# Kernel optimization log

Measured on AMD Instinct MI355X. Metric: run time of the kernel, lower is better.

## Reference

```python
import jax, jax.numpy as jnp
import numpy as np

D = 256; HEADS = 8; DH = D // HEADS; LEVELS = 4; POINTS = 4; NLAYERS = 6; DFF = 1024
SHAPES = ((92, 160), (46, 80), (23, 40), (12, 20))  # (H, W) per level
LEN = sum(h * w for h, w in SHAPES)  # 19560
BS = 4; NQ = 900; EPS = 1e-5
SCALE = 1.0 / float(np.sqrt(DH))


def setup_inputs() -> dict:
    ks = iter(jax.random.split(jax.random.key(0), 64))
    def rn(shape, s=0.02):
        return jax.random.normal(next(ks), shape, jnp.float32) * s
    inp = {}
    inp['tgt'] = jax.random.normal(next(ks), (BS, NQ, D), jnp.float32)
    inp['reference_points'] = jax.random.uniform(next(ks), (BS, NQ, 3), jnp.float32)
    inp['src'] = jax.random.normal(next(ks), (BS, LEN, D), jnp.float32)
    inp['valid_ratios'] = jnp.ones((BS, LEVELS, 2), jnp.float32)
    inp['query_pos'] = jax.random.normal(next(ks), (BS, NQ, D), jnp.float32)
    # per-layer stacked parameters [NLAYERS, ...]
    inp['sa_in_w'] = rn((NLAYERS, 3 * D, D)); inp['sa_in_b'] = jnp.zeros((NLAYERS, 3 * D))
    inp['sa_out_w'] = rn((NLAYERS, D, D)); inp['sa_out_b'] = jnp.zeros((NLAYERS, D))
    inp['samp_w'] = rn((NLAYERS, HEADS * LEVELS * POINTS * 2, D), 0.01)
    inp['samp_b'] = jax.random.uniform(next(ks), (NLAYERS, HEADS * LEVELS * POINTS * 2), jnp.float32, -2.0, 2.0)
    inp['attn_w'] = rn((NLAYERS, HEADS * LEVELS * POINTS, D)); inp['attn_b'] = jnp.zeros((NLAYERS, HEADS * LEVELS * POINTS))
    inp['val_w'] = rn((NLAYERS, D, D)); inp['val_b'] = jnp.zeros((NLAYERS, D))
    inp['ca_out_w'] = rn((NLAYERS, D, D)); inp['ca_out_b'] = jnp.zeros((NLAYERS, D))
    inp['ffn1_w'] = rn((NLAYERS, DFF, D)); inp['ffn1_b'] = jnp.zeros((NLAYERS, DFF))
    inp['ffn2_w'] = rn((NLAYERS, D, DFF)); inp['ffn2_b'] = jnp.zeros((NLAYERS, D))
    for i in (1, 2, 3):
        inp['ln%d_w' % i] = jnp.ones((NLAYERS, D)); inp['ln%d_b' % i] = jnp.zeros((NLAYERS, D))
    return inp


def _ln(x, w, b):
    mu = x.mean(-1, keepdims=True)
    var = ((x - mu) ** 2).mean(-1, keepdims=True)
    return (x - mu) / jnp.sqrt(var + EPS) * w + b


def _self_attn(q, k, v, in_w, in_b, out_w, out_b):
    wq, wk, wv = jnp.split(in_w, 3, 0)
    bq, bk, bv = jnp.split(in_b, 3, 0)
    def proj(x, w, b):
        return (x @ w.T + b).reshape(BS, -1, HEADS, DH).transpose(0, 2, 1, 3)
    qh, kh, vh = proj(q, wq, bq), proj(k, wk, bk), proj(v, wv, bv)
    att = jax.nn.softmax(jnp.einsum('bhqd,bhkd->bhqk', qh * SCALE, kh), axis=-1)
    o = jnp.einsum('bhqk,bhkd->bhqd', att, vh).transpose(0, 2, 1, 3).reshape(BS, -1, D)
    return o @ out_w.T + out_b


def _msda(query, ref, src, sw, sb, aw, ab, vw, vb, ow, ob):
    # query [bs,NQ,D]; ref [bs,NQ,LEVELS,2] normalized xz coords
    value = (src @ vw.T + vb).reshape(BS, LEN, HEADS, DH)
    off = (query @ sw.T + sb).reshape(BS, NQ, HEADS, LEVELS, POINTS, 2)
    attn = jax.nn.softmax((query @ aw.T + ab).reshape(BS, NQ, HEADS, LEVELS * POINTS), -1)
    attn = attn.reshape(BS, NQ, HEADS, LEVELS, POINTS)
    norm = jnp.asarray([[w, h] for h, w in SHAPES], jnp.float32)  # (W,H) per level
    loc = ref[:, :, None, :, None, :] + off / norm[None, None, None, :, None, :]
    out = jnp.zeros((BS, HEADS, NQ, DH), jnp.float32)
    start = 0
    for l, (H, W) in enumerate(SHAPES):
        v_l = value[:, start:start + H * W].transpose(0, 2, 1, 3)  # [bs,heads,HW,dh]
        start += H * W
        ll = loc[:, :, :, l]  # [bs,NQ,heads,P,2]
        x = ll[..., 0] * W - 0.5
        y = ll[..., 1] * H - 0.5
        x0 = jnp.floor(x); y0 = jnp.floor(y)
        fx = x - x0; fy = y - y0
        x0i = x0.astype(jnp.int32); y0i = y0.astype(jnp.int32)
        def gather(xi, yi):
            inb = ((xi >= 0) & (xi < W) & (yi >= 0) & (yi < H)).astype(jnp.float32)
            idx = jnp.clip(yi, 0, H - 1) * W + jnp.clip(xi, 0, W - 1)
            idxt = idx.transpose(0, 2, 1, 3).reshape(BS, HEADS, NQ * POINTS, 1)
            g = jnp.take_along_axis(v_l, idxt, axis=2).reshape(BS, HEADS, NQ, POINTS, DH)
            return g * inb.transpose(0, 2, 1, 3)[..., None]
        def wt(w4):
            return w4.transpose(0, 2, 1, 3)[..., None]
        samp = (gather(x0i, y0i) * wt((1 - fx) * (1 - fy))
                + gather(x0i + 1, y0i) * wt(fx * (1 - fy))
                + gather(x0i, y0i + 1) * wt((1 - fx) * fy)
                + gather(x0i + 1, y0i + 1) * wt(fx * fy))
        out = out + (samp * attn[:, :, :, l].transpose(0, 2, 1, 3)[..., None]).sum(3)
    out = out.transpose(0, 2, 1, 3).reshape(BS, NQ, D)
    return out @ ow.T + ob


def _forward(tgt, reference_points, src, valid_ratios, query_pos,
             sa_in_w, sa_in_b, sa_out_w, sa_out_b,
             samp_w, samp_b, attn_w, attn_b, val_w, val_b, ca_out_w, ca_out_b,
             ffn1_w, ffn1_b, ffn2_w, ffn2_b,
             ln1_w, ln1_b, ln2_w, ln2_b, ln3_w, ln3_b):
    # reference_points last dim == 3 (x,y,z); deformable attn uses (x,z)
    ref_xz = jnp.concatenate([reference_points[..., :1], reference_points[..., 2:]], -1)
    ref_in = ref_xz[:, :, None] * valid_ratios[:, None]  # [bs,NQ,LEVELS,2]
    out = tgt
    for l in range(NLAYERS):
        q = out + query_pos
        sa = _self_attn(q, q, out, sa_in_w[l], sa_in_b[l], sa_out_w[l], sa_out_b[l])
        out = _ln(out + sa, ln1_w[l], ln1_b[l])
        ca = _msda(out + query_pos, ref_in, src, samp_w[l], samp_b[l], attn_w[l], attn_b[l],
                   val_w[l], val_b[l], ca_out_w[l], ca_out_b[l])
        out = _ln(out + ca, ln2_w[l], ln2_b[l])
        h = jax.nn.relu(out @ ffn1_w[l].T + ffn1_b[l]) @ ffn2_w[l].T + ffn2_b[l]
        out = _ln(out + h, ln3_w[l], ln3_b[l])
    return out


def reference(tgt, reference_points, src, valid_ratios, query_pos,
              sa_in_w, sa_in_b, sa_out_w, sa_out_b,
              samp_w, samp_b, attn_w, attn_b, val_w, val_b, ca_out_w, ca_out_b,
              ffn1_w, ffn1_b, ffn2_w, ffn2_b,
              ln1_w, ln1_b, ln2_w, ln2_b, ln3_w, ln3_b):
    return _forward(tgt, reference_points, src, valid_ratios, query_pos,
                    sa_in_w, sa_in_b, sa_out_w, sa_out_b,
                    samp_w, samp_b, attn_w, attn_b, val_w, val_b, ca_out_w, ca_out_b,
                    ffn1_w, ffn1_b, ffn2_w, ffn2_b,
                    ln1_w, ln1_b, ln2_w, ln2_b, ln3_w, ln3_b)
```

## Files before the change

kernel.cpp:

```cpp
#include <hip/hip_runtime.h>
#include <math.h>

#define DMODEL 256
#define HEADS 8
#define DHEAD 32
#define LEVELS 4
#define POINTS 4
#define NLAYERS 6
#define DFF 1024
#define BS 4
#define NQ 900
#define SLEN 19560
#define EPS_LN 1e-5f
#define ATT_SCALE 0.17677669529663689f

typedef __attribute__((ext_vector_type(8))) short bf16x8;
typedef __attribute__((ext_vector_type(4))) float f32x4;
typedef __attribute__((ext_vector_type(4))) unsigned short u16x4;
typedef __attribute__((ext_vector_type(8))) unsigned short u16x8;

__device__ __forceinline__ unsigned short f2b(float x) {
  unsigned u = __float_as_uint(x);
  u += 0x7FFF + ((u >> 16) & 1);
  return (unsigned short)(u >> 16);
}
__device__ __forceinline__ float b2f(unsigned short v) {
  return __uint_as_float(((unsigned)v) << 16);
}

__global__ __launch_bounds__(256) void copycvt_k(const float* __restrict__ a,
                                                 const float* __restrict__ qp,
                                                 float* __restrict__ cf,
                                                 unsigned short* __restrict__ cb,
                                                 unsigned short* __restrict__ qb, int n4) {
  int i = blockIdx.x * 256 + threadIdx.x;
  if (i < n4) {
    float4 v = reinterpret_cast<const float4*>(a)[i];
    float4 q = reinterpret_cast<const float4*>(qp)[i];
    reinterpret_cast<float4*>(cf)[i] = v;
    u16x4 o4 = {f2b(v.x), f2b(v.y), f2b(v.z), f2b(v.w)};
    reinterpret_cast<u16x4*>(cb)[i] = o4;
    u16x4 p4 = {f2b(q.x), f2b(q.y), f2b(q.z), f2b(q.w)};
    reinterpret_cast<u16x4*>(qb)[i] = p4;
  }
}

#define N4_SRC (SLEN * BS * DMODEL / 4)
#define N4_SAIN (NLAYERS * 768 * 256 / 4)
#define N4_SQ (NLAYERS * 256 * 256 / 4)
#define N4_FFN (NLAYERS * DFF * 256 / 4)
__global__ __launch_bounds__(256) void f2ball_k(
    const float* __restrict__ s0, const float* __restrict__ s1,
    const float* __restrict__ s2, const float* __restrict__ s3,
    const float* __restrict__ s4, const float* __restrict__ s5,
    const float* __restrict__ s6,
    unsigned short* __restrict__ d0, unsigned short* __restrict__ d1,
    unsigned short* __restrict__ d2, unsigned short* __restrict__ d3,
    unsigned short* __restrict__ d4, unsigned short* __restrict__ d5,
    unsigned short* __restrict__ d6) {
  const int total = N4_SRC + N4_SAIN + 3 * N4_SQ + 2 * N4_FFN;
  for (int i = blockIdx.x * 256 + threadIdx.x; i < total; i += gridDim.x * 256) {
    const float* s;
    unsigned short* d;
    int j = i;
    if (j < N4_SRC) { s = s0; d = d0; }
    else { j -= N4_SRC;
      if (j < N4_SAIN) { s = s1; d = d1; }
      else { j -= N4_SAIN;
        if (j < N4_SQ) { s = s2; d = d2; }
        else { j -= N4_SQ;
          if (j < N4_SQ) { s = s3; d = d3; }
          else { j -= N4_SQ;
            if (j < N4_SQ) { s = s4; d = d4; }
            else { j -= N4_SQ;
              if (j < N4_FFN) { s = s5; d = d5; }
              else { j -= N4_FFN; s = s6; d = d6; } } } } } }
    float4 v = reinterpret_cast<const float4*>(s)[j];
    u16x4 o4 = {f2b(v.x), f2b(v.y), f2b(v.z), f2b(v.w)};
    reinterpret_cast<u16x4*>(d)[j] = o4;
  }
}

__global__ __launch_bounds__(256) void catw_k(const float* __restrict__ sw,
                                              const float* __restrict__ aw,
                                              const float* __restrict__ sb,
                                              const float* __restrict__ ab,
                                              unsigned short* __restrict__ wout,
                                              float* __restrict__ bout) {
  int i = blockIdx.x * 256 + threadIdx.x;
  const int total4 = NLAYERS * 384 * 256 / 4;
  if (i < total4) {
    int l = i / (384 * 64);
    int r = i % (384 * 64);
    int row = r / 64;
    int c4 = r % 64;
    const float* srcp = row < 256
        ? sw + ((size_t)l * 256 * 256 + (size_t)row * 256 + c4 * 4)
        : aw + ((size_t)l * 128 * 256 + (size_t)(row - 256) * 256 + c4 * 4);
    float4 v = *(const float4*)srcp;
    u16x4 o4 = {f2b(v.x), f2b(v.y), f2b(v.z), f2b(v.w)};
    *(u16x4*)(wout + (size_t)i * 4) = o4;
  }
  if (i < NLAYERS * 384) {
    int l = i / 384, r = i % 384;
    bout[i] = r < 256 ? sb[l * 256 + r] : ab[l * 128 + (r - 256)];
  }
}

__global__ __launch_bounds__(256) void stackqk_k(const float* __restrict__ w_in,
                                                 const float* __restrict__ b_in,
                                                 unsigned short* __restrict__ qkW,
                                                 float* __restrict__ bqk) {
  int i = blockIdx.x * 256 + threadIdx.x;
  const int total4 = NLAYERS * 512 * 256 / 4;
  if (i < total4) {
    int l = i / (512 * 64);
    int r = i % (512 * 64);
    int row = r / 64, c4 = r % 64;
    float4 v = *(const float4*)(w_in + (size_t)l * 768 * 256 + (size_t)row * 256 + c4 * 4);
    u16x4 o4 = {f2b(v.x), f2b(v.y), f2b(v.z), f2b(v.w)};
    *(u16x4*)(qkW + ((size_t)(l * 512 + row) * 256 + c4 * 4)) = o4;
  }
  if (i < NLAYERS * 512) {
    int l = i / 512, r = i % 512;
    bqk[i] = b_in[l * 768 + r];
  }
}

__global__ __launch_bounds__(256) void gemm_bf_k(const unsigned short* __restrict__ A,
                                                 const unsigned short* __restrict__ W,
                                                 const float* __restrict__ bias,
                                                 const float* __restrict__ res,
                                                 int res_n, int ldr,
                                                 float* __restrict__ outf,
                                                 unsigned short* __restrict__ outb,
                                                 int ldo, int M, int N, int K, int relu) {
  __shared__ unsigned short As[64][72];
  __shared__ unsigned short Ws[64][72];
  const int tid = threadIdx.x;
  const int lane = tid & 63, wv = tid >> 6;
  const int wm = wv >> 1, wn = wv & 1;
  const int m0 = blockIdx.x * 64, n0 = blockIdx.y * 64;
  const int l15 = lane & 15, l4 = lane >> 4;

  f32x4 acc[2][2] = {};
  for (int k0 = 0; k0 < K; k0 += 64) {
#pragma unroll
    for (int t = 0; t < 2; ++t) {
      int u = t * 256 + tid;
      int r = u >> 3, c8 = u & 7;
      int ra = m0 + r; if (ra >= M) ra = M - 1;
      *(u16x8*)&As[r][c8 * 8] = *(const u16x8*)(A + (size_t)ra * K + k0 + c8 * 8);
      *(u16x8*)&Ws[r][c8 * 8] = *(const u16x8*)(W + (size_t)(n0 + r) * K + k0 + c8 * 8);
    }
    __syncthreads();
#pragma unroll
    for (int ks = 0; ks < 64; ks += 32) {
      bf16x8 af[2], wf[2];
#pragma unroll
      for (int fr = 0; fr < 2; ++fr)
        af[fr] = *(const bf16x8*)&As[wm * 32 + fr * 16 + l15][ks + l4 * 8];
#pragma unroll
      for (int fn = 0; fn < 2; ++fn)
        wf[fn] = *(const bf16x8*)&Ws[wn * 32 + fn * 16 + l15][ks + l4 * 8];
#pragma unroll
      for (int fr = 0; fr < 2; ++fr)
#pragma unroll
        for (int fn = 0; fn < 2; ++fn)
          acc[fr][fn] = __builtin_amdgcn_mfma_f32_16x16x32_bf16(
              af[fr], wf[fn], acc[fr][fn], 0, 0, 0);
    }
    __syncthreads();
  }
#pragma unroll
  for (int fr = 0; fr < 2; ++fr)
#pragma unroll
    for (int fn = 0; fn < 2; ++fn) {
      int col = n0 + wn * 32 + fn * 16 + l15;
      float bs = bias[col];
#pragma unroll
      for (int j = 0; j < 4; ++j) {
        int row = m0 + wm * 32 + fr * 16 + l4 * 4 + j;
        if (row >= M) continue;
        float v = acc[fr][fn][j];
        if (res && col < res_n) v += res[(size_t)row * ldr + col];
        else v += bs;
        if (relu) v = fmaxf(v, 0.f);
        if (outf) outf[(size_t)row * ldo + col] = v;
        if (outb) outb[(size_t)row * ldo + col] = f2b(v);
      }
    }
}

__global__ __launch_bounds__(256) void gemm_lnres_k(const unsigned short* __restrict__ A,
                                                    const unsigned short* __restrict__ W,
                                                    const float* __restrict__ bias,
                                                    const float* __restrict__ res,
                                                    const float* __restrict__ lnw,
                                                    const float* __restrict__ lnb,
                                                    float* __restrict__ outf,
                                                    unsigned short* __restrict__ outb,
                                                    int M, int K) {
  __shared__ unsigned short As[32][72];
  __shared__ unsigned short Ws[256][72];
  __shared__ float Os[32][264];
  const int tid = threadIdx.x;
  const int lane = tid & 63, wv = tid >> 6;
  const int l15 = lane & 15, l4 = lane >> 4;
  const int m0 = blockIdx.x * 32;

  f32x4 acc[2][4] = {};
  for (int k0 = 0; k0 < K; k0 += 64) {
    {
      int r = tid >> 3, c8 = tid & 7;
      int ra = m0 + r; if (ra >= M) ra = M - 1;
      *(u16x8*)&As[r][c8 * 8] = *(const u16x8*)(A + (size_t)ra * K + k0 + c8 * 8);
#pragma unroll
      for (int t = 0; t < 8; ++t) {
        int u = t * 256 + tid;
        int wr = u >> 3, wc = u & 7;
        *(u16x8*)&Ws[wr][wc * 8] = *(const u16x8*)(W + (size_t)wr * K + k0 + wc * 8);
      }
    }
    __syncthreads();
#pragma unroll
    for (int ks = 0; ks < 64; ks += 32) {
      bf16x8 af[2], wf[4];
#pragma unroll
      for (int fr = 0; fr < 2; ++fr)
        af[fr] = *(const bf16x8*)&As[fr * 16 + l15][ks + l4 * 8];
#pragma unroll
      for (int fc = 0; fc < 4; ++fc)
        wf[fc] = *(const bf16x8*)&Ws[wv * 64 + fc * 16 + l15][ks + l4 * 8];
#pragma unroll
      for (int fr = 0; fr < 2; ++fr)
#pragma unroll
        for (int fc = 0; fc < 4; ++fc)
          acc[fr][fc] = __builtin_amdgcn_mfma_f32_16x16x32_bf16(
              af[fr], wf[fc], acc[fr][fc], 0, 0, 0);
    }
    __syncthreads();
  }
#pragma unroll
  for (int fr = 0; fr < 2; ++fr)
#pragma unroll
    for (int fc = 0; fc < 4; ++fc) {
      int col = wv * 64 + fc * 16 + l15;
      float bs = bias[col];
#pragma unroll
      for (int j = 0; j < 4; ++j) {
        int row = fr * 16 + l4 * 4 + j;
        int grow = m0 + row;
        float v = acc[fr][fc][j] + bs + (grow < M ? res[(size_t)grow * 256 + col] : 0.f);
        Os[row][col] = v;
      }
    }
  __syncthreads();
  float4 wv4 = *(const float4*)(lnw + lane * 4);
  float4 bv4 = *(const float4*)(lnb + lane * 4);
#pragma unroll
  for (int i = 0; i < 8; ++i) {
    int row = wv * 8 + i;
    int grow = m0 + row;
    float4 x = *(float4*)&Os[row][lane * 4];
    float s = x.x + x.y + x.z + x.w;
#pragma unroll
    for (int m = 1; m < 64; m <<= 1) s += __shfl_xor(s, m);
    const float mu = s * (1.f / DMODEL);
    float4 v = {x.x - mu, x.y - mu, x.z - mu, x.w - mu};
    float q = v.x * v.x + v.y * v.y + v.z * v.z + v.w * v.w;
#pragma unroll
    for (int m = 1; m < 64; m <<= 1) q += __shfl_xor(q, m);
    const float rstd = rsqrtf(q * (1.f / DMODEL) + EPS_LN);
    float4 y = {v.x * rstd * wv4.x + bv4.x, v.y * rstd * wv4.y + bv4.y,
                v.z * rstd * wv4.z + bv4.z, v.w * rstd * wv4.w + bv4.w};
    if (grow < M) {
      *(float4*)(outf + (size_t)grow * 256 + lane * 4) = y;
      if (outb) {
        u16x4 ob = {f2b(y.x), f2b(y.y), f2b(y.z), f2b(y.w)};
        *(u16x4*)(outb + (size_t)grow * 256 + lane * 4) = ob;
      }
    }
  }
}

__global__ __launch_bounds__(256) void gemm_vmfma_k(const unsigned short* __restrict__ A,
                                                    const unsigned short* __restrict__ W,
                                                    const float* __restrict__ bias,
                                                    unsigned short* __restrict__ C,
                                                    int M) {
  __shared__ unsigned short As[128][72];
  __shared__ unsigned short Ws[128][72];
  const int tid = threadIdx.x;
  const int lane = tid & 63, wv = tid >> 6;
  const int wm = wv >> 1, wn = wv & 1;
  const int m0 = blockIdx.x * 128, n0 = blockIdx.y * 128;
  const int l15 = lane & 15, l4 = lane >> 4;

  f32x4 acc[4][4] = {};

  for (int k0 = 0; k0 < 256; k0 += 64) {
#pragma unroll
    for (int t = 0; t < 4; ++t) {
      int u = t * 256 + tid;
      int r = u >> 3, c8 = u & 7;
      int ra = m0 + r; if (ra >= M) ra = M - 1;
      *(u16x8*)&As[r][c8 * 8] = *(const u16x8*)(A + (size_t)ra * 256 + k0 + c8 * 8);
      *(u16x8*)&Ws[r][c8 * 8] = *(const u16x8*)(W + (size_t)(n0 + r) * 256 + k0 + c8 * 8);
    }
    __syncthreads();
#pragma unroll
    for (int ks = 0; ks < 64; ks += 32) {
      bf16x8 af[4], bf[4];
#pragma unroll
      for (int fr = 0; fr < 4; ++fr)
        af[fr] = *(const bf16x8*)&As[wm * 64 + fr * 16 + l15][ks + l4 * 8];
#pragma unroll
      for (int fn = 0; fn < 4; ++fn)
        bf[fn] = *(const bf16x8*)&Ws[wn * 64 + fn * 16 + l15][ks + l4 * 8];
#pragma unroll
      for (int fr = 0; fr < 4; ++fr)
#pragma unroll
        for (int fn = 0; fn < 4; ++fn)
          acc[fr][fn] = __builtin_amdgcn_mfma_f32_16x16x32_bf16(
              af[fr], bf[fn], acc[fr][fn], 0, 0, 0);
    }
    __syncthreads();
  }
#pragma unroll
  for (int fr = 0; fr < 4; ++fr)
#pragma unroll
    for (int fn = 0; fn < 4; ++fn) {
      int col = n0 + wn * 64 + fn * 16 + l15;
      float bs = bias[col];
#pragma unroll
      for (int j = 0; j < 4; ++j) {
        int row = m0 + wm * 64 + fr * 16 + l4 * 4 + j;
        if (row < M) C[(size_t)row * 256 + col] = f2b(acc[fr][fn][j] + bs);
      }
    }
}

__global__ __launch_bounds__(256) void fattn_mfma_k(const unsigned short* __restrict__ qkv,
                                                    unsigned short* __restrict__ o) {
  __shared__ unsigned short Qlds[64][40];
  __shared__ unsigned short Klds[64][40];
  __shared__ unsigned short Vt[32][72];
  __shared__ unsigned short Plds[64][72];
  const int tid = threadIdx.x;
  const int lane = tid & 63;
  const int wq = tid >> 6;
  const int l15 = lane & 15, l4 = lane >> 4;
  const int q0 = blockIdx.x * 64;
  const int h = blockIdx.y, b = blockIdx.z;
  const int hq = h * 32;
  const size_t rowb = (size_t)b * NQ;

  {
    int q = q0 + (tid >> 2);
    int qc = q < NQ ? q : NQ - 1;
    *(u16x8*)&Qlds[tid >> 2][(tid & 3) * 8] =
        *(const u16x8*)(qkv + (rowb + qc) * 768 + hq + (tid & 3) * 8);
  }
  __syncthreads();
  const bf16x8 qf = *(const bf16x8*)&Qlds[wq * 16 + l15][l4 * 8];

  float m_r[4] = {-1e30f, -1e30f, -1e30f, -1e30f};
  float l_r[4] = {0.f, 0.f, 0.f, 0.f};
  f32x4 oacc[2] = {};

  for (int k0 = 0; k0 < NQ; k0 += 64) {
    __syncthreads();
    {
      int kk = k0 + (tid >> 2);
      int kc = kk < NQ ? kk : NQ - 1;
      const unsigned short* kbase = qkv + (rowb + kc) * 768 + hq + (tid & 3) * 8;
      u16x8 kv = *(const u16x8*)(kbase + 256);
      u16x8 vv = *(const u16x8*)(kbase + 512);
      *(u16x8*)&Klds[tid >> 2][(tid & 3) * 8] = kv;
#pragma unroll
      for (int i = 0; i < 8; ++i) Vt[(tid & 3) * 8 + i][tid >> 2] = vv[i];
    }
    __syncthreads();

    f32x4 s[4];
#pragma unroll
    for (int fc = 0; fc < 4; ++fc) {
      bf16x8 kf = *(const bf16x8*)&Klds[fc * 16 + l15][l4 * 8];
      s[fc] = __builtin_amdgcn_mfma_f32_16x16x32_bf16(qf, kf, (f32x4){0.f, 0.f, 0.f, 0.f}, 0, 0, 0);
    }
#pragma unroll
    for (int fc = 0; fc < 4; ++fc) {
      bool oob = (k0 + fc * 16 + l15) >= NQ;
#pragma unroll
      for (int j = 0; j < 4; ++j)
        s[fc][j] = oob ? -1e30f : s[fc][j] * ATT_SCALE;
    }
#pragma unroll
    for (int j = 0; j < 4; ++j) {
      float tm = fmaxf(fmaxf(s[0][j], s[1][j]), fmaxf(s[2][j], s[3][j]));
      tm = fmaxf(tm, __shfl_xor(tm, 1, 16));
      tm = fmaxf(tm, __shfl_xor(tm, 2, 16));
      tm = fmaxf(tm, __shfl_xor(tm, 4, 16));
      tm = fmaxf(tm, __shfl_xor(tm, 8, 16));
      float mn = fmaxf(m_r[j], tm);
      float sf = __expf(m_r[j] - mn);
      m_r[j] = mn;
      oacc[0][j] *= sf;
      oacc[1][j] *= sf;
      float rs = 0.f;
#pragma unroll
      for (int fc = 0; fc < 4; ++fc) {
        float pv = __expf(s[fc][j] - mn);
        s[fc][j] = pv;
        rs += pv;
      }
      rs += __shfl_xor(rs, 1, 16);
      rs += __shfl_xor(rs, 2, 16);
      rs += __shfl_xor(rs, 4, 16);
      rs += __shfl_xor(rs, 8, 16);
      l_r[j] = l_r[j] * sf + rs;
    }
#pragma unroll
    for (int fc = 0; fc < 4; ++fc)
#pragma unroll
      for (int j = 0; j < 4; ++j)
        Plds[wq * 16 + l4 * 4 + j][fc * 16 + l15] = f2b(s[fc][j]);
    __syncthreads();
#pragma unroll
    for (int ks = 0; ks < 2; ++ks) {
      bf16x8 pf = *(const bf16x8*)&Plds[wq * 16 + l15][ks * 32 + l4 * 8];
#pragma unroll
      for (int oc = 0; oc < 2; ++oc) {
        bf16x8 vf = *(const bf16x8*)&Vt[oc * 16 + l15][ks * 32 + l4 * 8];
        oacc[oc] = __builtin_amdgcn_mfma_f32_16x16x32_bf16(pf, vf, oacc[oc], 0, 0, 0);
      }
    }
  }
#pragma unroll
  for (int j = 0; j < 4; ++j) {
    int q = q0 + wq * 16 + l4 * 4 + j;
    if (q < NQ) {
      float inv = 1.f / l_r[j];
      o[(rowb + q) * 256 + hq + l15] = f2b(oacc[0][j] * inv);
      o[(rowb + q) * 256 + hq + 16 + l15] = f2b(oacc[1][j] * inv);
    }
  }
}

__global__ __launch_bounds__(256) void msda_k(const float* __restrict__ refp,
                                              const float* __restrict__ vr,
                                              const unsigned short* __restrict__ value,
                                              const float* __restrict__ cat,
                                              unsigned short* __restrict__ outp) {
  const int HW[4][2] = {{92, 160}, {46, 80}, {23, 40}, {12, 20}};
  const int START[4] = {0, 14720, 18400, 19320};
  const int qi = blockIdx.x, b = blockIdx.y;
  const int tid = threadIdx.x;
  const int h = tid >> 5;
  const int r = tid & 31;
  const int lvl = r >> 3;
  const int li = r & 7;
  const size_t base = (size_t)(b * NQ + qi);
  const float rx = refp[base * 3 + 0];
  const float rz = refp[base * 3 + 2];

  const float* lg = cat + base * 384 + 256 + h * 16;
  float4 L0 = *(const float4*)(lg + 0);
  float4 L1 = *(const float4*)(lg + 4);
  float4 L2 = *(const float4*)(lg + 8);
  float4 L3 = *(const float4*)(lg + 12);
  float mx = fmaxf(fmaxf(fmaxf(L0.x, L0.y), fmaxf(L0.z, L0.w)),
                   fmaxf(fmaxf(fmaxf(L1.x, L1.y), fmaxf(L1.z, L1.w)),
                         fmaxf(fmaxf(fmaxf(L2.x, L2.y), fmaxf(L2.z, L2.w)),
                               fmaxf(fmaxf(L3.x, L3.y), fmaxf(L3.z, L3.w)))));
  float4 E0 = {__expf(L0.x - mx), __expf(L0.y - mx), __expf(L0.z - mx), __expf(L0.w - mx)};
  float4 E1 = {__expf(L1.x - mx), __expf(L1.y - mx), __expf(L1.z - mx), __expf(L1.w - mx)};
  float4 E2 = {__expf(L2.x - mx), __expf(L2.y - mx), __expf(L2.z - mx), __expf(L2.w - mx)};
  float4 E3 = {__expf(L3.x - mx), __expf(L3.y - mx), __expf(L3.z - mx), __expf(L3.w - mx)};
  float sum = E0.x + E0.y + E0.z + E0.w + E1.x + E1.y + E1.z + E1.w +
              E2.x + E2.y + E2.z + E2.w + E3.x + E3.y + E3.z + E3.w;
  const float inv = 1.f / sum;
  float4 Emy = lvl == 0 ? E0 : lvl == 1 ? E1 : lvl == 2 ? E2 : E3;
  float wl[4] = {Emy.x * inv, Emy.y * inv, Emy.z * inv, Emy.w * inv};

  const int H = HW[lvl][0], W = HW[lvl][1];
  const float refx = rx * vr[(b * LEVELS + lvl) * 2 + 0] * (float)W;
  const float refy = rz * vr[(b * LEVELS + lvl) * 2 + 1] * (float)H;
  const unsigned short* vbase = value + ((size_t)b * SLEN + START[lvl]) * DMODEL + h * DHEAD + li * 4;
  const float* ob = cat + base * 384 + h * 32 + lvl * 8;

  float a0 = 0.f, a1 = 0.f, a2 = 0.f, a3 = 0.f;
#pragma unroll
  for (int p = 0; p < 4; ++p) {
    const float x = refx + ob[p * 2 + 0] - 0.5f;
    const float y = refy + ob[p * 2 + 1] - 0.5f;
    const float x0f = floorf(x), y0f = floorf(y);
    const float fx = x - x0f, fy = y - y0f;
    const int x0 = (int)x0f, y0 = (int)y0f;
#pragma unroll
    for (int ci = 0; ci < 4; ++ci) {
      const int xi = x0 + (ci & 1);
      const int yi = y0 + (ci >> 1);
      if ((xi >= 0) && (xi < W) && (yi >= 0) && (yi < H)) {
        const float wxy = ((ci & 1) ? fx : 1.f - fx) * ((ci >> 1) ? fy : 1.f - fy) * wl[p];
        u16x4 v4 = *(const u16x4*)(vbase + (size_t)(yi * W + xi) * DMODEL);
        a0 = fmaf(wxy, b2f(v4[0]), a0);
        a1 = fmaf(wxy, b2f(v4[1]), a1);
        a2 = fmaf(wxy, b2f(v4[2]), a2);
        a3 = fmaf(wxy, b2f(v4[3]), a3);
      }
    }
  }
  a0 += __shfl_xor(a0, 8);  a1 += __shfl_xor(a1, 8);
  a2 += __shfl_xor(a2, 8);  a3 += __shfl_xor(a3, 8);
  a0 += __shfl_xor(a0, 16); a1 += __shfl_xor(a1, 16);
  a2 += __shfl_xor(a2, 16); a3 += __shfl_xor(a3, 16);
  if (lvl == 0) {
    u16x4 o4 = {f2b(a0), f2b(a1), f2b(a2), f2b(a3)};
    *(u16x4*)(outp + base * 256 + h * 32 + li * 4) = o4;
  }
}

extern "C" void kernel_launch(void* const* d_in, const int* in_sizes, int n_in,
                              void* d_out, int out_size, void* d_ws, size_t ws_size,
                              hipStream_t stream) {
  const float* tgt     = (const float*)d_in[0];
  const float* refp    = (const float*)d_in[1];
  const float* src     = (const float*)d_in[2];
  const float* vr      = (const float*)d_in[3];
  const float* qpos    = (const float*)d_in[4];
  const float* sa_in_w = (const float*)d_in[5];
  const float* sa_in_b = (const float*)d_in[6];
  const float* sa_out_w= (const float*)d_in[7];
  const float* sa_out_b= (const float*)d_in[8];
  const float* samp_w  = (const float*)d_in[9];
  const float* samp_b  = (const float*)d_in[10];
  const float* attn_w  = (const float*)d_in[11];
  const float* attn_b  = (const float*)d_in[12];
  const float* val_w   = (const float*)d_in[13];
  const float* val_b   = (const float*)d_in[14];
  const float* ca_out_w= (const float*)d_in[15];
  const float* ca_out_b= (const float*)d_in[16];
  const float* ffn1_w  = (const float*)d_in[17];
  const float* ffn1_b  = (const float*)d_in[18];
  const float* ffn2_w  = (const float*)d_in[19];
  const float* ffn2_b  = (const float*)d_in[20];
  const float* ln1_w   = (const float*)d_in[21];
  const float* ln1_b   = (const float*)d_in[22];
  const float* ln2_w   = (const float*)d_in[23];
  const float* ln2_b   = (const float*)d_in[24];
  const float* ln3_w   = (const float*)d_in[25];
  const float* ln3_b   = (const float*)d_in[26];

  const int M = BS * NQ;
  const int MV = BS * SLEN;
  const size_t TOK = (size_t)M * DMODEL;

  float* ws = (float*)d_ws;
  size_t off = 0;
  auto alloc = [&](size_t n) { float* p = ws + off; off += n; return p; };
  auto allocb = [&](size_t n) { unsigned short* p = (unsigned short*)(ws + off); off += (n + 1) / 2; return p; };
  float* cur     = alloc(TOK);
  float* catout  = alloc((size_t)M * 384);
  float* b_cacat = alloc((size_t)NLAYERS * 384);
  float* bqk     = alloc((size_t)NLAYERS * 512);
  float* qpos_qk = alloc((size_t)M * NLAYERS * 512);
  float* qpos_cat= alloc((size_t)M * NLAYERS * 384);
  unsigned short* cur_bf  = allocb(TOK);
  unsigned short* qpos_bf = allocb(TOK);
  unsigned short* sao_bf  = allocb(TOK);
  unsigned short* msda_bf = allocb(TOK);
  unsigned short* qkv_bf  = allocb((size_t)M * 768);
  unsigned short* ffnh_bf = allocb((size_t)M * DFF);
  unsigned short* src_bf  = allocb((size_t)MV * DMODEL);
  unsigned short* value_bf= allocb((size_t)MV * DMODEL);
  unsigned short* w_in_bf   = allocb((size_t)NLAYERS * 768 * 256);
  unsigned short* w_saout_bf= allocb((size_t)NLAYERS * 256 * 256);
  unsigned short* w_cacat_bf= allocb((size_t)NLAYERS * 384 * 256);
  unsigned short* w_val_bf  = allocb((size_t)NLAYERS * 256 * 256);
  unsigned short* w_caout_bf= allocb((size_t)NLAYERS * 256 * 256);
  unsigned short* w_ffn1_bf = allocb((size_t)NLAYERS * DFF * 256);
  unsigned short* w_ffn2_bf = allocb((size_t)NLAYERS * 256 * DFF);
  unsigned short* qkW_bf    = allocb((size_t)NLAYERS * 512 * 256);

  const int n4 = (int)(TOK / 4);
  const dim3 blk(256);
  const dim3 gE((n4 + 255) / 256);

  copycvt_k<<<gE, blk, 0, stream>>>(tgt, qpos, cur, cur_bf, qpos_bf, n4);
  f2ball_k<<<dim3(2048), blk, 0, stream>>>(src, sa_in_w, sa_out_w, val_w, ca_out_w,
                                           ffn1_w, ffn2_w,
                                           src_bf, w_in_bf, w_saout_bf, w_val_bf,
                                           w_caout_bf, w_ffn1_bf, w_ffn2_bf);
  catw_k<<<dim3(576), blk, 0, stream>>>(samp_w, attn_w, samp_b, attn_b, w_cacat_bf, b_cacat);
  stackqk_k<<<dim3(768), blk, 0, stream>>>(sa_in_w, sa_in_b, qkW_bf, bqk);
  gemm_bf_k<<<dim3(57, 48), blk, 0, stream>>>(qpos_bf, qkW_bf, bqk, nullptr, 0, 0,
                                              qpos_qk, nullptr, 3072, M, 3072, 256, 0);
  gemm_bf_k<<<dim3(57, 36), blk, 0, stream>>>(qpos_bf, w_cacat_bf, b_cacat, nullptr, 0, 0,
                                              qpos_cat, nullptr, 2304, M, 2304, 256, 0);

  const dim3 gQKV(57, 12);
  const dim3 gCat(57, 6);
  const dim3 gF1(57, 16);
  const dim3 gLN(113);

  for (int l = 0; l < NLAYERS; ++l) {
    gemm_bf_k<<<gQKV, blk, 0, stream>>>(cur_bf, w_in_bf + (size_t)l * 768 * 256,
                                        sa_in_b + l * 768,
                                        qpos_qk + (size_t)l * 512, 512, 3072,
                                        nullptr, qkv_bf, 768, M, 768, 256, 0);

    fattn_mfma_k<<<dim3((NQ + 63) / 64, HEADS, BS), blk, 0, stream>>>(qkv_bf, sao_bf);

    gemm_lnres_k<<<gLN, blk, 0, stream>>>(sao_bf, w_saout_bf + (size_t)l * 256 * 256,
                                          sa_out_b + l * 256, cur,
                                          ln1_w + l * 256, ln1_b + l * 256,
                                          cur, cur_bf, M, 256);

    gemm_vmfma_k<<<dim3((MV + 127) / 128, 2), blk, 0, stream>>>(
        src_bf, w_val_bf + (size_t)l * 256 * 256, val_b + l * 256, value_bf, MV);
    gemm_bf_k<<<gCat, blk, 0, stream>>>(cur_bf, w_cacat_bf + (size_t)l * 384 * 256,
                                        b_cacat + l * 384,
                                        qpos_cat + (size_t)l * 384, 384, 2304,
                                        catout, nullptr, 384, M, 384, 256, 0);

    msda_k<<<dim3(NQ, BS), blk, 0, stream>>>(refp, vr, value_bf, catout, msda_bf);

    gemm_lnres_k<<<gLN, blk, 0, stream>>>(msda_bf, w_caout_bf + (size_t)l * 256 * 256,
                                          ca_out_b + l * 256, cur,
                                          ln2_w + l * 256, ln2_b + l * 256,
                                          cur, cur_bf, M, 256);

    gemm_bf_k<<<gF1, blk, 0, stream>>>(cur_bf, w_ffn1_bf + (size_t)l * DFF * 256,
                                       ffn1_b + l * DFF, nullptr, 0, 0,
                                       nullptr, ffnh_bf, DFF, M, DFF, 256, 1);
    const bool last = (l == NLAYERS - 1);
    gemm_lnres_k<<<gLN, blk, 0, stream>>>(ffnh_bf, w_ffn2_bf + (size_t)l * 256 * DFF,
                                          ffn2_b + l * 256, cur,
                                          ln3_w + l * 256, ln3_b + l * 256,
                                          last ? (float*)d_out : cur,
                                          last ? nullptr : cur_bf, M, DFF);
  }
}
```

Before: 1.407 ms.

## Fuse query_pos add into LayerNorm epilogue and drop precomputed qpos projections

Instead of precomputing query_pos projections for all layers (large fp32 buffers read as residuals in each GEMM epilogue), the LN-residual GEMM epilogue now also writes a bf16 copy of (out + query_pos). The QKV GEMM reads that buffer for the Q/K columns and cur_bf for the V columns, and the sampling/attention-weight GEMM reads it directly. This removes two large upfront GEMMs, the stackqk conversion, and the fp32 residual reads. The LN-residual GEMM tile also shrinks from 32 to 16 rows, doubling the grid, at the cost of reloading the full weight tile more often.

```diff
diff --git a/kernel.cpp b/kernel.cpp
--- a/kernel.cpp
+++ b/kernel.cpp
@@ -40,7 +40,7 @@
     reinterpret_cast<float4*>(cf)[i] = v;
     u16x4 o4 = {f2b(v.x), f2b(v.y), f2b(v.z), f2b(v.w)};
     reinterpret_cast<u16x4*>(cb)[i] = o4;
-    u16x4 p4 = {f2b(q.x), f2b(q.y), f2b(q.z), f2b(q.w)};
+    u16x4 p4 = {f2b(v.x + q.x), f2b(v.y + q.y), f2b(v.z + q.z), f2b(v.w + q.w)};
     reinterpret_cast<u16x4*>(qb)[i] = p4;
   }
 }
@@ -107,31 +107,11 @@
   }
 }
 
-__global__ __launch_bounds__(256) void stackqk_k(const float* __restrict__ w_in,
-                                                 const float* __restrict__ b_in,
-                                                 unsigned short* __restrict__ qkW,
-                                                 float* __restrict__ bqk) {
-  int i = blockIdx.x * 256 + threadIdx.x;
-  const int total4 = NLAYERS * 512 * 256 / 4;
-  if (i < total4) {
-    int l = i / (512 * 64);
-    int r = i % (512 * 64);
-    int row = r / 64, c4 = r % 64;
-    float4 v = *(const float4*)(w_in + (size_t)l * 768 * 256 + (size_t)row * 256 + c4 * 4);
-    u16x4 o4 = {f2b(v.x), f2b(v.y), f2b(v.z), f2b(v.w)};
-    *(u16x4*)(qkW + ((size_t)(l * 512 + row) * 256 + c4 * 4)) = o4;
-  }
-  if (i < NLAYERS * 512) {
-    int l = i / 512, r = i % 512;
-    bqk[i] = b_in[l * 768 + r];
-  }
-}
-
 __global__ __launch_bounds__(256) void gemm_bf_k(const unsigned short* __restrict__ A,
+                                                 const unsigned short* __restrict__ A2,
+                                                 int nsplit,
                                                  const unsigned short* __restrict__ W,
                                                  const float* __restrict__ bias,
-                                                 const float* __restrict__ res,
-                                                 int res_n, int ldr,
                                                  float* __restrict__ outf,
                                                  unsigned short* __restrict__ outb,
                                                  int ldo, int M, int N, int K, int relu) {
@@ -142,6 +122,7 @@
   const int wm = wv >> 1, wn = wv & 1;
   const int m0 = blockIdx.x * 64, n0 = blockIdx.y * 64;
   const int l15 = lane & 15, l4 = lane >> 4;
+  const unsigned short* __restrict__ Ause = (n0 >= nsplit) ? A2 : A;
 
   f32x4 acc[2][2] = {};
   for (int k0 = 0; k0 < K; k0 += 64) {
@@ -150,7 +131,7 @@
       int u = t * 256 + tid;
       int r = u >> 3, c8 = u & 7;
       int ra = m0 + r; if (ra >= M) ra = M - 1;
-      *(u16x8*)&As[r][c8 * 8] = *(const u16x8*)(A + (size_t)ra * K + k0 + c8 * 8);
+      *(u16x8*)&As[r][c8 * 8] = *(const u16x8*)(Ause + (size_t)ra * K + k0 + c8 * 8);
       *(u16x8*)&Ws[r][c8 * 8] = *(const u16x8*)(W + (size_t)(n0 + r) * K + k0 + c8 * 8);
     }
     __syncthreads();
@@ -182,9 +163,7 @@
       for (int j = 0; j < 4; ++j) {
         int row = m0 + wm * 32 + fr * 16 + l4 * 4 + j;
         if (row >= M) continue;
-        float v = acc[fr][fn][j];
-        if (res && col < res_n) v += res[(size_t)row * ldr + col];
-        else v += bs;
+        float v = acc[fr][fn][j] + bs;
         if (relu) v = fmaxf(v, 0.f);
         if (outf) outf[(size_t)row * ldo + col] = v;
         if (outb) outb[(size_t)row * ldo + col] = f2b(v);
@@ -198,69 +177,61 @@
                                                     const float* __restrict__ res,
                                                     const float* __restrict__ lnw,
                                                     const float* __restrict__ lnb,
+                                                    const float* __restrict__ qpos,
                                                     float* __restrict__ outf,
                                                     unsigned short* __restrict__ outb,
+                                                    unsigned short* __restrict__ qposb,
                                                     int M, int K) {
-  __shared__ unsigned short As[32][72];
+  __shared__ unsigned short As[16][72];
   __shared__ unsigned short Ws[256][72];
-  __shared__ float Os[32][264];
+  __shared__ float Os[16][264];
   const int tid = threadIdx.x;
   const int lane = tid & 63, wv = tid >> 6;
   const int l15 = lane & 15, l4 = lane >> 4;
-  const int m0 = blockIdx.x * 32;
-
-  f32x4 acc[2][4] = {};
+  const int m0 = blockIdx.x * 16;
+
+  f32x4 acc[4] = {};
   for (int k0 = 0; k0 < K; k0 += 64) {
-    {
+    if (tid < 128) {
       int r = tid >> 3, c8 = tid & 7;
       int ra = m0 + r; if (ra >= M) ra = M - 1;
       *(u16x8*)&As[r][c8 * 8] = *(const u16x8*)(A + (size_t)ra * K + k0 + c8 * 8);
-#pragma unroll
-      for (int t = 0; t < 8; ++t) {
-        int u = t * 256 + tid;
-        int wr = u >> 3, wc = u & 7;
-        *(u16x8*)&Ws[wr][wc * 8] = *(const u16x8*)(W + (size_t)wr * K + k0 + wc * 8);
-      }
+    }
+#pragma unroll
+    for (int t = 0; t < 8; ++t) {
+      int u = t * 256 + tid;
+      int wr = u >> 3, wc = u & 7;
+      *(u16x8*)&Ws[wr][wc * 8] = *(const u16x8*)(W + (size_t)wr * K + k0 + wc * 8);
     }
     __syncthreads();
 #pragma unroll
     for (int ks = 0; ks < 64; ks += 32) {
-      bf16x8 af[2], wf[4];
-#pragma unroll
-      for (int fr = 0; fr < 2; ++fr)
-        af[fr] = *(const bf16x8*)&As[fr * 16 + l15][ks + l4 * 8];
-#pragma unroll
-      for (int fc = 0; fc < 4; ++fc)
-        wf[fc] = *(const bf16x8*)&Ws[wv * 64 + fc * 16 + l15][ks + l4 * 8];
-#pragma unroll
-      for (int fr = 0; fr < 2; ++fr)
-#pragma unroll
-        for (int fc = 0; fc < 4; ++fc)
-          acc[fr][fc] = __builtin_amdgcn_mfma_f32_16x16x32_bf16(
-              af[fr], wf[fc], acc[fr][fc], 0, 0, 0);
-    }
-    __syncthreads();
-  }
-#pragma unroll
-  for (int fr = 0; fr < 2; ++fr)
-#pragma unroll
-    for (int fc = 0; fc < 4; ++fc) {
-      int col = wv * 64 + fc * 16 + l15;
-      float bs = bias[col];
-#pragma unroll
-      for (int j = 0; j < 4; ++j) {
-        int row = fr * 16 + l4 * 4 + j;
-        int grow = m0 + row;
-        float v = acc[fr][fc][j] + bs + (grow < M ? res[(size_t)grow * 256 + col] : 0.f);
-        Os[row][col] = v;
-      }
-    }
+      bf16x8 af = *(const bf16x8*)&As[l15][ks + l4 * 8];
+#pragma unroll
+      for (int fc = 0; fc < 4; ++fc) {
+        bf16x8 wf = *(const bf16x8*)&Ws[wv * 64 + fc * 16 + l15][ks + l4 * 8];
+        acc[fc] = __builtin_amdgcn_mfma_f32_16x16x32_bf16(af, wf, acc[fc], 0, 0, 0);
+      }
+    }
+    __syncthreads();
+  }
+#pragma unroll
+  for (int fc = 0; fc < 4; ++fc) {
+    int col = wv * 64 + fc * 16 + l15;
+    float bs = bias[col];
+#pragma unroll
+    for (int j = 0; j < 4; ++j) {
+      int row = l4 * 4 + j;
+      int grow = m0 + row;
+      Os[row][col] = acc[fc][j] + bs + (grow < M ? res[(size_t)grow * 256 + col] : 0.f);
+    }
+  }
   __syncthreads();
   float4 wv4 = *(const float4*)(lnw + lane * 4);
   float4 bv4 = *(const float4*)(lnb + lane * 4);
 #pragma unroll
-  for (int i = 0; i < 8; ++i) {
-    int row = wv * 8 + i;
+  for (int i = 0; i < 4; ++i) {
+    int row = wv * 4 + i;
     int grow = m0 + row;
     float4 x = *(float4*)&Os[row][lane * 4];
     float s = x.x + x.y + x.z + x.w;
@@ -279,6 +250,11 @@
       if (outb) {
         u16x4 ob = {f2b(y.x), f2b(y.y), f2b(y.z), f2b(y.w)};
         *(u16x4*)(outb + (size_t)grow * 256 + lane * 4) = ob;
+      }
+      if (qposb) {
+        float4 qv = *(const float4*)(qpos + (size_t)grow * 256 + lane * 4);
+        u16x4 ob = {f2b(y.x + qv.x), f2b(y.y + qv.y), f2b(y.z + qv.z), f2b(y.w + qv.w)};
+        *(u16x4*)(qposb + (size_t)grow * 256 + lane * 4) = ob;
       }
     }
   }
@@ -564,11 +540,8 @@
   float* cur     = alloc(TOK);
   float* catout  = alloc((size_t)M * 384);
   float* b_cacat = alloc((size_t)NLAYERS * 384);
-  float* bqk     = alloc((size_t)NLAYERS * 512);
-  float* qpos_qk = alloc((size_t)M * NLAYERS * 512);
-  float* qpos_cat= alloc((size_t)M * NLAYERS * 384);
   unsigned short* cur_bf  = allocb(TOK);
-  unsigned short* qpos_bf = allocb(TOK);
+  unsigned short* qbuf_bf = allocb(TOK);
   unsigned short* sao_bf  = allocb(TOK);
   unsigned short* msda_bf = allocb(TOK);
   unsigned short* qkv_bf  = allocb((size_t)M * 768);
@@ -582,64 +555,62 @@
   unsigned short* w_caout_bf= allocb((size_t)NLAYERS * 256 * 256);
   unsigned short* w_ffn1_bf = allocb((size_t)NLAYERS * DFF * 256);
   unsigned short* w_ffn2_bf = allocb((size_t)NLAYERS * 256 * DFF);
-  unsigned short* qkW_bf    = allocb((size_t)NLAYERS * 512 * 256);
 
   const int n4 = (int)(TOK / 4);
   const dim3 blk(256);
   const dim3 gE((n4 + 255) / 256);
 
-  copycvt_k<<<gE, blk, 0, stream>>>(tgt, qpos, cur, cur_bf, qpos_bf, n4);
+  copycvt_k<<<gE, blk, 0, stream>>>(tgt, qpos, cur, cur_bf, qbuf_bf, n4);
   f2ball_k<<<dim3(2048), blk, 0, stream>>>(src, sa_in_w, sa_out_w, val_w, ca_out_w,
                                            ffn1_w, ffn2_w,
                                            src_bf, w_in_bf, w_saout_bf, w_val_bf,
                                            w_caout_bf, w_ffn1_bf, w_ffn2_bf);
   catw_k<<<dim3(576), blk, 0, stream>>>(samp_w, attn_w, samp_b, attn_b, w_cacat_bf, b_cacat);
-  stackqk_k<<<dim3(768), blk, 0, stream>>>(sa_in_w, sa_in_b, qkW_bf, bqk);
-  gemm_bf_k<<<dim3(57, 48), blk, 0, stream>>>(qpos_bf, qkW_bf, bqk, nullptr, 0, 0,
-                                              qpos_qk, nullptr, 3072, M, 3072, 256, 0);
-  gemm_bf_k<<<dim3(57, 36), blk, 0, stream>>>(qpos_bf, w_cacat_bf, b_cacat, nullptr, 0, 0,
-                                              qpos_cat, nullptr, 2304, M, 2304, 256, 0);
-
+
+  const int BIG = 1 << 30;
   const dim3 gQKV(57, 12);
   const dim3 gCat(57, 6);
   const dim3 gF1(57, 16);
-  const dim3 gLN(113);
+  const dim3 gLN(225);
 
   for (int l = 0; l < NLAYERS; ++l) {
-    gemm_bf_k<<<gQKV, blk, 0, stream>>>(cur_bf, w_in_bf + (size_t)l * 768 * 256,
+    gemm_bf_k<<<gQKV, blk, 0, stream>>>(qbuf_bf, cur_bf, 512,
+                                        w_in_bf + (size_t)l * 768 * 256,
                                         sa_in_b + l * 768,
-                                        qpos_qk + (size_t)l * 512, 512, 3072,
                                         nullptr, qkv_bf, 768, M, 768, 256, 0);
 
     fattn_mfma_k<<<dim3((NQ + 63) / 64, HEADS, BS), blk, 0, stream>>>(qkv_bf, sao_bf);
 
     gemm_lnres_k<<<gLN, blk, 0, stream>>>(sao_bf, w_saout_bf + (size_t)l * 256 * 256,
                                           sa_out_b + l * 256, cur,
-                                          ln1_w + l * 256, ln1_b + l * 256,
-                                          cur, cur_bf, M, 256);
+                                          ln1_w + l * 256, ln1_b + l * 256, qpos,
+                                          cur, nullptr, qbuf_bf, M, 256);
 
     gemm_vmfma_k<<<dim3((MV + 127) / 128, 2), blk, 0, stream>>>(
         src_bf, w_val_bf + (size_t)l * 256 * 256, val_b + l * 256, value_bf, MV);
-    gemm_bf_k<<<gCat, blk, 0, stream>>>(cur_bf, w_cacat_bf + (size_t)l * 384 * 256,
+    gemm_bf_k<<<gCat, blk, 0, stream>>>(qbuf_bf, qbuf_bf, BIG,
+                                        w_cacat_bf + (size_t)l * 384 * 256,
                                         b_cacat + l * 384,
-                                        qpos_cat + (size_t)l * 384, 384, 2304,
                                         catout, nullptr, 384, M, 384, 256, 0);
 
     msda_k<<<dim3(NQ, BS), blk, 0, stream>>>(refp, vr, value_bf, catout, msda_bf);
 
     gemm_lnres_k<<<gLN, blk, 0, stream>>>(msda_bf, w_caout_bf + (size_t)l * 256 * 256,
                                           ca_out_b + l * 256, cur,
-                                          ln2_w + l * 256, ln2_b + l * 256,
-                                          cur, cur_bf, M, 256);
-
-    gemm_bf_k<<<gF1, blk, 0, stream>>>(cur_bf, w_ffn1_bf + (size_t)l * DFF * 256,
-                                       ffn1_b + l * DFF, nullptr, 0, 0,
+                                          ln2_w + l * 256, ln2_b + l * 256, nullptr,
+                                          cur, cur_bf, nullptr, M, 256);
+
+    gemm_bf_k<<<gF1, blk, 0, stream>>>(cur_bf, cur_bf, BIG,
+                                       w_ffn1_bf + (size_t)l * DFF * 256,
+                                       ffn1_b + l * DFF,
                                        nullptr, ffnh_bf, DFF, M, DFF, 256, 1);
     const bool last = (l == NLAYERS - 1);
     gemm_lnres_k<<<gLN, blk, 0, stream>>>(ffnh_bf, w_ffn2_bf + (size_t)l * 256 * DFF,
                                           ffn2_b + l * 256, cur,
                                           ln3_w + l * 256, ln3_b + l * 256,
+                                          last ? nullptr : qpos,
                                           last ? (float*)d_out : cur,
-                                          last ? nullptr : cur_bf, M, DFF);
-  }
-}
+                                          last ? nullptr : cur_bf,
+                                          last ? nullptr : qbuf_bf, M, DFF);
+  }
+}
```

Result: faster. 1.226 ms (-12.8%).
